# Optimization experiments

Hardware: AMD Instinct MI355X
Metric: run time of the kernel (lower is better)

Reference implementation:

```python
import jax, jax.numpy as jnp
import numpy as np

# Human3.6M 17-joint skeleton (parent of each joint; -1 = root)
_PARENTS = np.array([-1, 0, 1, 2, 0, 4, 5, 0, 7, 8, 9, 8, 11, 12, 8, 14, 15])
J = 17          # joints
C_OUT = 128     # out_features (per-channel adjacency count)
F_IN = 128      # in_features
B, T = 64, 243  # batch, frames
NEG = -9.0e15   # matches torch constant -9000000000000000.0


def _skeleton_indices():
    A = np.eye(J, dtype=np.float32)  # self-loops (SemGCN adjacency includes I)
    for i, p in enumerate(_PARENTS):
        if p >= 0:
            A[i, p] = 1.0
            A[p, i] = 1.0
    ii, jj = np.nonzero(A)  # row-major order, identical to torch adj>0 mask order
    return ii.astype(np.int32), jj.astype(np.int32)


def setup_inputs() -> dict:
    key = jax.random.key(0)
    kx, kw, ke = jax.random.split(key, 3)
    ii, jj = _skeleton_indices()  # nnz = 49
    x = jax.random.normal(kx, (B, T, J, F_IN), dtype=jnp.float32)
    # xavier_uniform with gain=1.414 over (2, in, out)
    bound = 1.414 * np.sqrt(6.0 / (F_IN + C_OUT))
    W = jax.random.uniform(kw, (2, F_IN, C_OUT), dtype=jnp.float32,
                           minval=-bound, maxval=bound)
    e = jax.random.uniform(ke, (C_OUT, ii.shape[0]), dtype=jnp.float32)
    return {"x": x, "W": W, "e": e,
            "idx_i": jnp.asarray(ii), "idx_j": jnp.asarray(jj)}


def reference(x, W, e, idx_i, idx_j):
    # x: [B,T,J,F_in], W: [2,F_in,C], e: [C,nnz]
    C = e.shape[0]
    nj = x.shape[2]
    h0 = jnp.einsum('btji,io->btjo', x, W[0])  # [B,T,J,C]
    h1 = jnp.einsum('btji,io->btjo', x, W[1])  # [B,T,J,C]
    # dense per-channel adjacency: masked scatter of e, then row softmax
    adj = jnp.full((C, nj, nj), NEG, dtype=x.dtype)
    adj = adj.at[:, idx_i, idx_j].set(e)
    adj = jax.nn.softmax(adj, axis=2)  # [C,J,J]
    # diagonal part: (adj*E) @ h0  ==  elementwise scale by diag entries
    d = jnp.diagonal(adj, axis1=1, axis2=2)        # [C,J]
    eye = jnp.eye(nj, dtype=x.dtype)
    off = adj * (1.0 - eye)                         # [C,J,J]
    out = h0 * d.T[None, None] + jnp.einsum('cjk,btkc->btjc', off, h1)
    return out  # [B,T,J,C]
```

## Files before the change

### kernel.cpp

```cpp
#include <hip/hip_runtime.h>

#define NJ   17
#define FD   128
#define NC   128
#define NNZ  49
#define FPT  16
#define XROW (NJ*FD)
#define WS_WT 65536

typedef __attribute__((ext_vector_type(8))) short bf16x8;
typedef __attribute__((ext_vector_type(4))) float f32x4;

__device__ __forceinline__ ushort f2bf(float f) {
  unsigned u = __float_as_uint(f);
  u = (u + 0x7fffu + ((u >> 16) & 1u)) >> 16;
  return (ushort)u;
}
__device__ __forceinline__ float bf2f(ushort s) {
  return __uint_as_float(((unsigned)s) << 16);
}
__device__ __forceinline__ unsigned cvtpk(float a, float b) {
  unsigned r;
  asm("v_cvt_pk_bf16_f32 %0, %1, %2" : "=v"(r) : "v"(a), "v"(b));
  return r;
}
__device__ __forceinline__ bf16x8 pack8(float4 a, float4 b) {
  union { unsigned u[4]; bf16x8 v; } r;
  r.u[0] = cvtpk(a.x, a.y); r.u[1] = cvtpk(a.z, a.w);
  r.u[2] = cvtpk(b.x, b.y); r.u[3] = cvtpk(b.z, b.w);
  return r.v;
}
__device__ __forceinline__ void axpy(f32x4& o, float s, f32x4 h) {
  o[0] += s * h[0]; o[1] += s * h[1]; o[2] += s * h[2]; o[3] += s * h[3];
}

struct CI { int col, dk, n, jl[3], kk[3]; };
constexpr CI TAB0[9] = {
  {0,  0, 3, {1,4,7}, {4,12,20}},
  {1,  5, 2, {0,2,0}, {1,7,0}},
  {2,  8, 2, {1,3,0}, {6,10,0}},
  {3, 11, 1, {2,0,0}, {9,0,0}},
  {4, 13, 2, {0,5,0}, {2,15,0}},
  {5, 16, 2, {4,6,0}, {14,18,0}},
  {6, 19, 1, {5,0,0}, {17,0,0}},
  {7, 21, 1, {0,0,0}, {3,0,0}},
  {8, -1, 1, {7,0,0}, {22,0,0}},
};
constexpr CI TAB1[10] = {
  {7, -1, 1, {0,0,0}, {23,0,0}},
  {8, 24, 3, {1,3,6}, {28,33,41}},
  {9, 29, 2, {0,2,0}, {25,31,0}},
  {10,32, 1, {1,0,0}, {30,0,0}},
  {11,34, 2, {0,4,0}, {26,36,0}},
  {12,37, 2, {3,5,0}, {35,39,0}},
  {13,40, 1, {4,0,0}, {38,0,0}},
  {14,42, 2, {0,7,0}, {27,44,0}},
  {15,45, 2, {6,8,0}, {43,47,0}},
  {16,48, 1, {7,0,0}, {46,0,0}},
};
constexpr int RP[NJ + 1] = {0,4,7,10,12,15,18,20,23,28,31,33,36,39,41,44,47,49};

__global__ void prep_pack_kernel(const float* __restrict__ W,
                                 const float* __restrict__ e,
                                 bf16x8* __restrict__ Wpack,
                                 ushort* __restrict__ wt) {
  const int tid = threadIdx.x;
  if (blockIdx.x < 16) {
    const int idx = blockIdx.x * 256 + tid, n = idx >> 4, kb = idx & 15;
    const float* Wp = W + (size_t)(n >> 7) * (FD * NC) + (n & 127);
    bf16x8 v;
#pragma unroll
    for (int q = 0; q < 8; ++q) v[q] = (short)f2bf(Wp[(size_t)(kb * 8 + q) * NC]);
    Wpack[idx] = v;
  } else if (tid < NC) {
    const int c = tid;
    for (int j = 0; j < NJ; ++j) {
      const int k0 = RP[j], k1 = RP[j + 1];
      float m = -1e30f;
      for (int k = k0; k < k1; ++k) m = fmaxf(m, e[c * NNZ + k]);
      float s = 0.f;
      for (int k = k0; k < k1; ++k) s += expf(e[c * NNZ + k] - m);
      const float inv = 1.f / s;
      for (int k = k0; k < k1; ++k) wt[c * 64 + k] = f2bf(expf(e[c * NNZ + k] - m) * inv);
    }
    for (int k = NNZ; k < 64; ++k) wt[c * 64 + k] = 0;
  }
}

template <int HALF>
__device__ __forceinline__ void half_work(const float* __restrict__ xt,
                                          float* __restrict__ ob,
                                          const bf16x8* __restrict__ Wpack,
                                          const ushort* __restrict__ wt,
                                          short* xs, int tid) {
  constexpr int COL0 = HALF ? 7 : 0;
  constexpr int NCOL = HALF ? 10 : 9;
  constexpr int JN   = HALF ? 9 : 8;
  constexpr int JB   = HALF ? 8 : 0;
  constexpr int NCI  = HALF ? 10 : 9;
  constexpr int NGRP = FPT * NCOL * 16;
  const CI* TT = HALF ? TAB1 : TAB0;

  const int w = tid >> 6, lane = tid & 63, l15 = lane & 15, l4 = lane >> 4;
  const int cb = w * 16;
  const int c  = cb + l15;

  float4 v[10];
#pragma unroll
  for (int i = 0; i < 5; ++i) {
    const int g = tid + i * 512;
    if (NGRP % 512 == 0 || g < NGRP) {
      const int fr = g / (NCOL * 16), rem = g - fr * (NCOL * 16);
      const float* sp = xt + (size_t)fr * XROW + COL0 * FD + rem * 8;
      v[2 * i]     = *(const float4*)(sp);
      v[2 * i + 1] = *(const float4*)(sp + 4);
    }
  }

  bf16x8 bfr[2][4];
#pragma unroll
  for (int sel = 0; sel < 2; ++sel)
#pragma unroll
    for (int ks = 0; ks < 4; ++ks)
      bfr[sel][ks] = Wpack[(sel * 128 + c) * 16 + ks * 4 + l4];
  bf16x8 wtp[7];
#pragma unroll
  for (int r = 0; r < 7; ++r)
    wtp[r] = *(const bf16x8*)(wt + c * 64 + r * 8);

#pragma unroll
  for (int i = 0; i < 5; ++i) {
    const int g = tid + i * 512;
    if (NGRP % 512 == 0 || g < NGRP) {
      const int fr = g / (NCOL * 16);
      const int byte = (g * 16) ^ ((fr & 7) << 4);
      *(bf16x8*)((char*)xs + byte) = pack8(v[2 * i], v[2 * i + 1]);
    }
  }
  __syncthreads();

  f32x4 oa[JN];
#pragma unroll
  for (int j = 0; j < JN; ++j) oa[j] = (f32x4){0.f, 0.f, 0.f, 0.f};

#pragma unroll
  for (int ci = 0; ci < NCI; ++ci) {
    const int lc = TT[ci].col - COL0, dk = TT[ci].dk, nn = TT[ci].n;
    bf16x8 af[4];
#pragma unroll
    for (int ks = 0; ks < 4; ++ks) {
      const int byte = l15 * (NCOL * 256) + lc * 256 +
                       (((ks * 4 + l4) * 16) ^ ((l15 & 7) << 4));
      af[ks] = *(const bf16x8*)((const char*)xs + byte);
    }
    f32x4 h1 = (f32x4){0.f, 0.f, 0.f, 0.f};
#pragma unroll
    for (int ks = 0; ks < 4; ++ks)
      h1 = __builtin_amdgcn_mfma_f32_16x16x32_bf16(af[ks], bfr[1][ks], h1, 0, 0, 0);
    if (dk >= 0) {
      f32x4 h0 = (f32x4){0.f, 0.f, 0.f, 0.f};
#pragma unroll
      for (int ks = 0; ks < 4; ++ks)
        h0 = __builtin_amdgcn_mfma_f32_16x16x32_bf16(af[ks], bfr[0][ks], h0, 0, 0, 0);
      axpy(oa[TT[ci].col - JB], bf2f((ushort)wtp[dk >> 3][dk & 7]), h0);
    }
#pragma unroll
    for (int o = 0; o < 3; ++o)
      if (o < nn)
        axpy(oa[TT[ci].jl[o]], bf2f((ushort)wtp[TT[ci].kk[o] >> 3][TT[ci].kk[o] & 7]), h1);
  }

#pragma unroll
  for (int j = 0; j < JN; ++j)
#pragma unroll
    for (int q = 0; q < 4; ++q)
      ob[(size_t)(l4 * 4 + q) * XROW + (JB + j) * FD + c] = oa[j][q];
}

__global__ __launch_bounds__(512, 4) void fused_kernel(
    const float*  __restrict__ x,
    const bf16x8* __restrict__ Wpack,
    const ushort* __restrict__ wt,
    float*        __restrict__ out) {
  __shared__ __align__(16) short xs[FPT * 10 * FD];
  const int tile = blockIdx.x >> 1;
  const float* xt = x + (size_t)tile * (FPT * XROW);
  float* ob = out + (size_t)tile * (FPT * XROW);
  if (blockIdx.x & 1) half_work<1>(xt, ob, Wpack, wt, xs, threadIdx.x);
  else                half_work<0>(xt, ob, Wpack, wt, xs, threadIdx.x);
}

extern "C" void kernel_launch(void* const* d_in, const int* in_sizes, int n_in,
                              void* d_out, int out_size, void* d_ws, size_t ws_size,
                              hipStream_t stream) {
  const float* x = (const float*)d_in[0];
  const float* W = (const float*)d_in[1];
  const float* e = (const float*)d_in[2];
  float* out = (float*)d_out;

  bf16x8* Wpack = (bf16x8*)d_ws;
  ushort* wt    = (ushort*)((char*)d_ws + WS_WT);

  prep_pack_kernel<<<17, 256, 0, stream>>>(W, e, Wpack, wt);

  const int frames = in_sizes[0] / XROW;
  const int ntiles = frames / FPT;
  fused_kernel<<<ntiles * 2, 512, 0, stream>>>(x, Wpack, wt, out);
}
```

Baseline: 99.81 us.

## Warp-specialize fused kernel with producer waves double-buffering x tiles in LDS

Replaces the two-half-per-block design with persistent blocks that process four 16-frame tiles each. Four extra producer waves load and convert the next tile to bf16 into a second LDS buffer while eight consumer waves run MFMAs on the current one. Each block now covers all 17 joints, which removes the duplicated column-7 loads and the recomputed h1. Outputs are stored as soon as each joint's accumulator is final. The cost is fewer blocks (ntiles/4, which requires ntiles to be divisible by 4), larger LDS use per block, and more registers per thread at 768 threads.

```diff
diff --git a/kernel.cpp b/kernel.cpp
--- a/kernel.cpp
+++ b/kernel.cpp
@@ -6,6 +6,8 @@
 #define NNZ  49
 #define FPT  16
 #define XROW (NJ*FD)
+#define TPB  4
+#define TILEB (NJ*FPT*FD*2)
 #define WS_WT 65536
 
 typedef __attribute__((ext_vector_type(8))) short bf16x8;
@@ -34,29 +36,33 @@
   o[0] += s * h[0]; o[1] += s * h[1]; o[2] += s * h[2]; o[3] += s * h[3];
 }
 
-struct CI { int col, dk, n, jl[3], kk[3]; };
-constexpr CI TAB0[9] = {
-  {0,  0, 3, {1,4,7}, {4,12,20}},
-  {1,  5, 2, {0,2,0}, {1,7,0}},
-  {2,  8, 2, {1,3,0}, {6,10,0}},
-  {3, 11, 1, {2,0,0}, {9,0,0}},
-  {4, 13, 2, {0,5,0}, {2,15,0}},
-  {5, 16, 2, {4,6,0}, {14,18,0}},
-  {6, 19, 1, {5,0,0}, {17,0,0}},
-  {7, 21, 1, {0,0,0}, {3,0,0}},
-  {8, -1, 1, {7,0,0}, {22,0,0}},
+#define BARR() do { asm volatile("s_waitcnt lgkmcnt(0)" ::: "memory"); \
+                    __builtin_amdgcn_s_barrier(); \
+                    __builtin_amdgcn_sched_barrier(0); } while (0)
+
+struct CIM { int dk, n, jl[4], kk[4]; };
+constexpr CIM TABM[NJ] = {
+  {0,  3, {1,4,7,0},   {4,12,20,0}},
+  {5,  2, {0,2,0,0},   {1,7,0,0}},
+  {8,  2, {1,3,0,0},   {6,10,0,0}},
+  {11, 1, {2,0,0,0},   {9,0,0,0}},
+  {13, 2, {0,5,0,0},   {2,15,0,0}},
+  {16, 2, {4,6,0,0},   {14,18,0,0}},
+  {19, 1, {5,0,0,0},   {17,0,0,0}},
+  {21, 2, {0,8,0,0},   {3,23,0,0}},
+  {24, 4, {7,9,11,14}, {22,28,33,41}},
+  {29, 2, {8,10,0,0},  {25,31,0,0}},
+  {32, 1, {9,0,0,0},   {30,0,0,0}},
+  {34, 2, {8,12,0,0},  {26,36,0,0}},
+  {37, 2, {11,13,0,0}, {35,39,0,0}},
+  {40, 1, {12,0,0,0},  {38,0,0,0}},
+  {42, 2, {8,15,0,0},  {27,44,0,0}},
+  {45, 2, {14,16,0,0}, {43,47,0,0}},
+  {48, 1, {15,0,0,0},  {46,0,0,0}},
 };
-constexpr CI TAB1[10] = {
-  {7, -1, 1, {0,0,0}, {23,0,0}},
-  {8, 24, 3, {1,3,6}, {28,33,41}},
-  {9, 29, 2, {0,2,0}, {25,31,0}},
-  {10,32, 1, {1,0,0}, {30,0,0}},
-  {11,34, 2, {0,4,0}, {26,36,0}},
-  {12,37, 2, {3,5,0}, {35,39,0}},
-  {13,40, 1, {4,0,0}, {38,0,0}},
-  {14,42, 2, {0,7,0}, {27,44,0}},
-  {15,45, 2, {6,8,0}, {43,47,0}},
-  {16,48, 1, {7,0,0}, {46,0,0}},
+constexpr int FLM[NJ][2] = {
+  {-1,-1},{-1,-1},{1,-1},{2,3},{-1,-1},{4,-1},{5,6},{0,-1},{7,-1},
+  {-1,-1},{9,10},{-1,-1},{11,-1},{12,13},{8,-1},{14,-1},{15,16}
 };
 constexpr int RP[NJ + 1] = {0,4,7,10,12,15,18,20,23,28,31,33,36,39,41,44,47,49};
 
@@ -87,107 +93,119 @@
   }
 }
 
-template <int HALF>
-__device__ __forceinline__ void half_work(const float* __restrict__ xt,
-                                          float* __restrict__ ob,
-                                          const bf16x8* __restrict__ Wpack,
-                                          const ushort* __restrict__ wt,
-                                          short* xs, int tid) {
-  constexpr int COL0 = HALF ? 7 : 0;
-  constexpr int NCOL = HALF ? 10 : 9;
-  constexpr int JN   = HALF ? 9 : 8;
-  constexpr int JB   = HALF ? 8 : 0;
-  constexpr int NCI  = HALF ? 10 : 9;
-  constexpr int NGRP = FPT * NCOL * 16;
-  const CI* TT = HALF ? TAB1 : TAB0;
-
-  const int w = tid >> 6, lane = tid & 63, l15 = lane & 15, l4 = lane >> 4;
-  const int cb = w * 16;
-  const int c  = cb + l15;
-
-  float4 v[10];
-#pragma unroll
-  for (int i = 0; i < 5; ++i) {
-    const int g = tid + i * 512;
-    if (NGRP % 512 == 0 || g < NGRP) {
-      const int fr = g / (NCOL * 16), rem = g - fr * (NCOL * 16);
-      const float* sp = xt + (size_t)fr * XROW + COL0 * FD + rem * 8;
-      v[2 * i]     = *(const float4*)(sp);
-      v[2 * i + 1] = *(const float4*)(sp + 4);
-    }
-  }
-
-  bf16x8 bfr[2][4];
-#pragma unroll
-  for (int sel = 0; sel < 2; ++sel)
-#pragma unroll
-    for (int ks = 0; ks < 4; ++ks)
-      bfr[sel][ks] = Wpack[(sel * 128 + c) * 16 + ks * 4 + l4];
-  bf16x8 wtp[7];
-#pragma unroll
-  for (int r = 0; r < 7; ++r)
-    wtp[r] = *(const bf16x8*)(wt + c * 64 + r * 8);
-
-#pragma unroll
-  for (int i = 0; i < 5; ++i) {
-    const int g = tid + i * 512;
-    if (NGRP % 512 == 0 || g < NGRP) {
-      const int fr = g / (NCOL * 16);
-      const int byte = (g * 16) ^ ((fr & 7) << 4);
-      *(bf16x8*)((char*)xs + byte) = pack8(v[2 * i], v[2 * i + 1]);
-    }
-  }
-  __syncthreads();
-
-  f32x4 oa[JN];
-#pragma unroll
-  for (int j = 0; j < JN; ++j) oa[j] = (f32x4){0.f, 0.f, 0.f, 0.f};
-
-#pragma unroll
-  for (int ci = 0; ci < NCI; ++ci) {
-    const int lc = TT[ci].col - COL0, dk = TT[ci].dk, nn = TT[ci].n;
-    bf16x8 af[4];
-#pragma unroll
-    for (int ks = 0; ks < 4; ++ks) {
-      const int byte = l15 * (NCOL * 256) + lc * 256 +
-                       (((ks * 4 + l4) * 16) ^ ((l15 & 7) << 4));
-      af[ks] = *(const bf16x8*)((const char*)xs + byte);
-    }
-    f32x4 h1 = (f32x4){0.f, 0.f, 0.f, 0.f};
-#pragma unroll
-    for (int ks = 0; ks < 4; ++ks)
-      h1 = __builtin_amdgcn_mfma_f32_16x16x32_bf16(af[ks], bfr[1][ks], h1, 0, 0, 0);
-    if (dk >= 0) {
-      f32x4 h0 = (f32x4){0.f, 0.f, 0.f, 0.f};
-#pragma unroll
-      for (int ks = 0; ks < 4; ++ks)
-        h0 = __builtin_amdgcn_mfma_f32_16x16x32_bf16(af[ks], bfr[0][ks], h0, 0, 0, 0);
-      axpy(oa[TT[ci].col - JB], bf2f((ushort)wtp[dk >> 3][dk & 7]), h0);
-    }
-#pragma unroll
-    for (int o = 0; o < 3; ++o)
-      if (o < nn)
-        axpy(oa[TT[ci].jl[o]], bf2f((ushort)wtp[TT[ci].kk[o] >> 3][TT[ci].kk[o] & 7]), h1);
-  }
-
-#pragma unroll
-  for (int j = 0; j < JN; ++j)
-#pragma unroll
-    for (int q = 0; q < 4; ++q)
-      ob[(size_t)(l4 * 4 + q) * XROW + (JB + j) * FD + c] = oa[j][q];
-}
-
-__global__ __launch_bounds__(512, 4) void fused_kernel(
+__global__ __launch_bounds__(768, 3) void fused_kernel(
     const float*  __restrict__ x,
     const bf16x8* __restrict__ Wpack,
     const ushort* __restrict__ wt,
     float*        __restrict__ out) {
-  __shared__ __align__(16) short xs[FPT * 10 * FD];
-  const int tile = blockIdx.x >> 1;
-  const float* xt = x + (size_t)tile * (FPT * XROW);
-  float* ob = out + (size_t)tile * (FPT * XROW);
-  if (blockIdx.x & 1) half_work<1>(xt, ob, Wpack, wt, xs, threadIdx.x);
-  else                half_work<0>(xt, ob, Wpack, wt, xs, threadIdx.x);
+  __shared__ __align__(16) char xs[2 * TILEB];
+  const int tid = threadIdx.x;
+  const int wid = tid >> 6;
+  const int t0  = blockIdx.x * TPB;
+
+  if (wid >= 8) {
+    const int p = tid - 512;
+    float4 a[12];
+
+#define PLOAD(T, K) do {                                                    \
+      const int g_ = p + (K) * 256;                                         \
+      const int fr_ = g_ / (NJ * 16), rem_ = g_ - fr_ * (NJ * 16);          \
+      const float* s_ = x + ((size_t)(T) * FPT + fr_) * XROW + rem_ * 8;    \
+      a[((K) % 6) * 2]     = *(const float4*)s_;                            \
+      a[((K) % 6) * 2 + 1] = *(const float4*)(s_ + 4);                      \
+    } while (0)
+#define PWRITE(BUF, K) do {                                                 \
+      const int g_ = p + (K) * 256;                                         \
+      const int fr_ = g_ / (NJ * 16);                                       \
+      const int byte_ = (g_ * 16) ^ ((fr_ & 7) << 4);                       \
+      *(bf16x8*)((BUF) + byte_) = pack8(a[((K) % 6) * 2],                   \
+                                        a[((K) % 6) * 2 + 1]);              \
+    } while (0)
+#define PSTAGE(T, BUF) do {                                                 \
+      PLOAD(T,0); PLOAD(T,1); PLOAD(T,2); PLOAD(T,3); PLOAD(T,4); PLOAD(T,5);\
+      PWRITE(BUF,0);  PLOAD(T,6);  PWRITE(BUF,1);  PLOAD(T,7);              \
+      PWRITE(BUF,2);  PLOAD(T,8);  PWRITE(BUF,3);  PLOAD(T,9);              \
+      PWRITE(BUF,4);  PLOAD(T,10); PWRITE(BUF,5);  PLOAD(T,11);             \
+      PWRITE(BUF,6);  PLOAD(T,12); PWRITE(BUF,7);  PLOAD(T,13);             \
+      PWRITE(BUF,8);  PLOAD(T,14); PWRITE(BUF,9);  PLOAD(T,15);             \
+      PWRITE(BUF,10); PLOAD(T,16); PWRITE(BUF,11); PWRITE(BUF,12);          \
+      PWRITE(BUF,13); PWRITE(BUF,14); PWRITE(BUF,15); PWRITE(BUF,16);       \
+    } while (0)
+
+    PSTAGE(t0, xs);
+    BARR();
+#pragma unroll
+    for (int i = 0; i < TPB; ++i) {
+      if (i + 1 < TPB) PSTAGE(t0 + i + 1, xs + ((i + 1) & 1) * TILEB);
+      BARR();
+    }
+#undef PSTAGE
+#undef PWRITE
+#undef PLOAD
+  } else {
+    const int lane = tid & 63, l15 = lane & 15, l4 = lane >> 4;
+    const int c = wid * 16 + l15;
+
+    bf16x8 bfr[2][4];
+#pragma unroll
+    for (int sel = 0; sel < 2; ++sel)
+#pragma unroll
+      for (int ks = 0; ks < 4; ++ks)
+        bfr[sel][ks] = Wpack[(sel * 128 + c) * 16 + ks * 4 + l4];
+    bf16x8 wtp[7];
+#pragma unroll
+    for (int r = 0; r < 7; ++r)
+      wtp[r] = *(const bf16x8*)(wt + c * 64 + r * 8);
+
+    BARR();
+
+#pragma unroll
+    for (int i = 0; i < TPB; ++i) {
+      const char* cur = xs + (i & 1) * TILEB;
+      float* const ob = out + (size_t)(t0 + i) * (FPT * XROW);
+
+      f32x4 oa[NJ];
+#pragma unroll
+      for (int j = 0; j < NJ; ++j) oa[j] = (f32x4){0.f, 0.f, 0.f, 0.f};
+
+#pragma unroll
+      for (int ci = 0; ci < NJ; ++ci) {
+        const int dk = TABM[ci].dk, nn = TABM[ci].n;
+        bf16x8 af[4];
+#pragma unroll
+        for (int ks = 0; ks < 4; ++ks) {
+          const int byte = l15 * (NJ * 256) + ci * 256 +
+                           (((ks * 4 + l4) * 16) ^ ((l15 & 7) << 4));
+          af[ks] = *(const bf16x8*)(cur + byte);
+        }
+        f32x4 h1 = (f32x4){0.f, 0.f, 0.f, 0.f};
+#pragma unroll
+        for (int ks = 0; ks < 4; ++ks)
+          h1 = __builtin_amdgcn_mfma_f32_16x16x32_bf16(af[ks], bfr[1][ks], h1, 0, 0, 0);
+        f32x4 h0 = (f32x4){0.f, 0.f, 0.f, 0.f};
+#pragma unroll
+        for (int ks = 0; ks < 4; ++ks)
+          h0 = __builtin_amdgcn_mfma_f32_16x16x32_bf16(af[ks], bfr[0][ks], h0, 0, 0, 0);
+        axpy(oa[ci], bf2f((ushort)wtp[dk >> 3][dk & 7]), h0);
+#pragma unroll
+        for (int o = 0; o < 4; ++o)
+          if (o < nn)
+            axpy(oa[TABM[ci].jl[o]],
+                 bf2f((ushort)wtp[TABM[ci].kk[o] >> 3][TABM[ci].kk[o] & 7]), h1);
+
+#pragma unroll
+        for (int fi = 0; fi < 2; ++fi) {
+          const int fj = FLM[ci][fi];
+          if (fj >= 0) {
+#pragma unroll
+            for (int q = 0; q < 4; ++q)
+              ob[(size_t)(l4 * 4 + q) * XROW + fj * FD + c] = oa[fj][q];
+          }
+        }
+      }
+      BARR();
+    }
+  }
 }
 
 extern "C" void kernel_launch(void* const* d_in, const int* in_sizes, int n_in,
@@ -205,5 +223,6 @@
 
   const int frames = in_sizes[0] / XROW;
   const int ntiles = frames / FPT;
-  fused_kernel<<<ntiles * 2, 512, 0, stream>>>(x, Wpack, wt, out);
-}
+  const int blocks = ntiles / TPB;
+  fused_kernel<<<blocks, 768, 0, stream>>>(x, Wpack, wt, out);
+}
```

New measurement: 121.9 us. +22.2%, slower.
